# Performance work log

Hardware: AMD Instinct MI355X
Metric: run time of the kernel (lower is better)

Reference implementation:

```python
import jax, jax.numpy as jnp
import numpy as np

N, M, D, H = 16, 1024, 64, 4  # batch, num_node, dim_in==dim_hid, num_head
NEG_SLOPE = 0.2


def setup_inputs() -> dict:
    key = jax.random.key(0)
    ks = jax.random.split(key, 10)
    s = 1.0 / np.sqrt(D)
    inp = {
        "x": jax.random.normal(ks[0], (N, M, D), dtype=jnp.float32),
        "edge": jnp.zeros((N, M, M), dtype=jnp.float32),  # unused by the module
        # stacked per-head Linear(dim_in, dim_hid) params: weight (H, D_out, D_in), bias (H, D_out)
        "Wk": (jax.random.normal(ks[1], (H, D, D), dtype=jnp.float32) * s),
        "bk": (jax.random.normal(ks[2], (H, D), dtype=jnp.float32) * s),
        "Wq": (jax.random.normal(ks[3], (H, D, D), dtype=jnp.float32) * s),
        "bq": (jax.random.normal(ks[4], (H, D), dtype=jnp.float32) * s),
        "Wv": (jax.random.normal(ks[5], (H, D, D), dtype=jnp.float32) * s),
        "bv": (jax.random.normal(ks[6], (H, D), dtype=jnp.float32) * s),
        # decoder: Linear(dim_hid*num_head -> dim_in)
        "Wdec": (jax.random.normal(ks[7], (D, H * D), dtype=jnp.float32) / np.sqrt(H * D)),
        "bdec": (jax.random.normal(ks[8], (D,), dtype=jnp.float32) / np.sqrt(H * D)),
    }
    return inp


def reference(x, edge, Wk, bk, Wq, bq, Wv, bv, Wdec, bdec):
    # x: (N, M, D). Per head h: K = x @ Wk[h].T + bk[h], etc.
    K = jnp.einsum("nmd,hed->nhme", x, Wk) + bk[None, :, None, :]  # (N,H,M,D)
    Q = jnp.einsum("nmd,hed->nhme", x, Wq) + bq[None, :, None, :]
    V = jnp.einsum("nmd,hed->nhme", x, Wv) + bv[None, :, None, :]
    # alpha[n,h,i,j] = K[n,h,i] . Q[n,h,j]  (sender=K row i, receiver=Q row j)
    alpha = jnp.einsum("nhie,nhje->nhij", K, Q)  # (N,H,M,M)
    alpha = jax.nn.leaky_relu(alpha, NEG_SLOPE)
    alpha = jax.nn.softmax(alpha, axis=-1)
    agg = jnp.einsum("nhij,nhje->nhie", alpha, V)  # (N,H,M,D)
    dx = jax.nn.leaky_relu(agg, NEG_SLOPE) - x[:, None, :, :]  # (N,H,M,D)
    # concat heads along feature dim (head 0 first): (N, M, H*D)
    dx = dx.transpose(0, 2, 1, 3).reshape(N, M, H * D)
    return dx @ Wdec.T + bdec  # (N, M, D)
```

## Files before the change

### kernel.cpp

```cpp
#include <hip/hip_runtime.h>
#include <hip/hip_bf16.h>


#define NB 16
#define MM 1024
#define DD 64
#define HH 4
#define NEG 0.2f
#define AST 72
#define DST 264
#define LOG2E 1.44269504088896f

typedef __attribute__((ext_vector_type(8))) short bf16x8;
typedef __attribute__((ext_vector_type(8))) _Float16 f16x8;
typedef __attribute__((ext_vector_type(16))) float f32x16;
typedef __attribute__((ext_vector_type(4))) unsigned int uint4v;
typedef __attribute__((ext_vector_type(2))) unsigned int uint2v;

__device__ inline unsigned short f2bf(float f) {
  unsigned int u = __builtin_bit_cast(unsigned int, f);
  unsigned int r = (u + 0x7FFFu + ((u >> 16) & 1u)) >> 16;
  return (unsigned short)r;
}
__device__ inline unsigned short f2h(float f) {
  _Float16 h = (_Float16)f;
  return __builtin_bit_cast(unsigned short, h);
}
__device__ inline unsigned int pk_bf16(float lo, float hi) {
  unsigned int r;
  asm("v_cvt_pk_bf16_f32 %0, %1, %2" : "=v"(r) : "v"(lo), "v"(hi));
  return r;
}
__device__ inline void swap32(unsigned int& a, unsigned int& b) {
  uint2v r = __builtin_amdgcn_permlane32_swap(a, b, false, false);
  a = r.x;
  b = r.y;
}

__global__ __launch_bounds__(256) void prep_kernel(
    const float* __restrict__ Wk, const float* __restrict__ Wq,
    const float* __restrict__ Wv, const float* __restrict__ Wdec,
    unsigned short* __restrict__ Wf) {
  const int idx = (blockIdx.x * 256 + threadIdx.x) * 4;
  const int seg = idx >> 14, local = idx & 16383;
  const float* src = seg == 0 ? Wk : seg == 1 ? Wq : seg == 2 ? Wv : Wdec;
  float4 v = *(const float4*)&src[local];
  unsigned short p[4] = {f2h(v.x), f2h(v.y), f2h(v.z), f2h(v.w)};
  *(uint2*)&Wf[idx] = *(uint2*)p;
}

__global__ __launch_bounds__(256) void proj_kernel(
    const float* __restrict__ x, const unsigned short* __restrict__ Wf,
    const float* __restrict__ bk, const float* __restrict__ bq, const float* __restrict__ bv,
    unsigned short* __restrict__ Kf, unsigned short* __restrict__ Qf,
    unsigned short* __restrict__ Vtg) {
  __shared__ unsigned short xs[64 * AST];
  __shared__ unsigned short ob[64 * AST];
  const int t = threadIdx.x;
  const int r0 = blockIdx.x * 64;
  const int combo = blockIdx.y, mat = combo >> 2, h = combo & 3;
  const int n = r0 >> 10, ml = r0 & 1023;
  const float* bias = mat == 0 ? bk : (mat == 1 ? bq : bv);

#pragma unroll
  for (int rep = 0; rep < 2; ++rep) {
    int idx = rep * 256 + t, row = idx >> 3, c8 = (idx & 7) * 8;
    float4 a = *(const float4*)&x[(size_t)(r0 + row) * DD + c8];
    float4 b = *(const float4*)&x[(size_t)(r0 + row) * DD + c8 + 4];
    unsigned short p[8] = {f2h(a.x), f2h(a.y), f2h(a.z), f2h(a.w),
                           f2h(b.x), f2h(b.y), f2h(b.z), f2h(b.w)};
    *(uint4*)&xs[row * AST + c8] = *(uint4*)p;
  }
  __syncthreads();

  const int w = t >> 6, lane = t & 63, m31 = lane & 31, hf = lane >> 5;
  const int mi = w >> 1, ne = w & 1;
  const int ecol = h * 64 + ne * 32 + m31;
  const float bb = bias[ecol];

  f32x16 C;
#pragma unroll
  for (int r = 0; r < 16; ++r) C[r] = 0.f;
#pragma unroll
  for (int ks = 0; ks < 4; ++ks) {
    f16x8 xa = *(f16x8*)&xs[(mi * 32 + m31) * AST + ks * 16 + hf * 8];
    f16x8 wb = *(const f16x8*)&Wf[(size_t)mat * 16384 + (size_t)ecol * DD + ks * 16 + hf * 8];
    C = __builtin_amdgcn_mfma_f32_32x32x16_f16(xa, wb, C, 0, 0, 0);
  }

  if (mat < 2) {
    const float ksc = (mat == 0) ? LOG2E : 1.0f;
#pragma unroll
    for (int r = 0; r < 16; ++r) {
      int rr = (r & 3) + 8 * (r >> 2) + 4 * hf;
      ob[(mi * 32 + rr) * AST + ne * 32 + m31] = f2h((C[r] + bb) * ksc);
    }
  } else {
#pragma unroll
    for (int r = 0; r < 16; ++r) {
      int rr = (r & 3) + 8 * (r >> 2) + 4 * hf;
      ob[(ne * 32 + m31) * AST + mi * 32 + rr] = f2bf(C[r] + bb);
    }
  }
  __syncthreads();

  if (mat < 2) {
    unsigned short* dst = mat == 0 ? Kf : Qf;
    const size_t obase = (((size_t)n * HH + h) * MM + ml) * DD;
#pragma unroll
    for (int rep = 0; rep < 2; ++rep) {
      int idx = rep * 256 + t, row = idx >> 3, c8 = (idx & 7) * 8;
      *(uint4*)&dst[obase + (size_t)row * DD + c8] = *(uint4*)&ob[row * AST + c8];
    }
  } else {
    const size_t obase = (((size_t)n * HH + h) * DD) * MM + ml;
#pragma unroll
    for (int rep = 0; rep < 2; ++rep) {
      int idx = rep * 256 + t, row = idx >> 3, c8 = (idx & 7) * 8;
      *(uint4*)&Vtg[obase + (size_t)row * MM + c8] = *(uint4*)&ob[row * AST + c8];
    }
  }
}

__global__ __launch_bounds__(256, 2) void attn_kernel(
    const unsigned short* __restrict__ Kf, const unsigned short* __restrict__ Qf,
    const unsigned short* __restrict__ Vtg, const float* __restrict__ x,
    unsigned short* __restrict__ DX) {
  __shared__ __align__(16) unsigned short sm[4 * 64 * AST];
  __shared__ float ls[128];

  const int t = threadIdx.x;
  const int w = t >> 6, lane = t & 63;
  const int m31 = lane & 31, hf = lane >> 5;

  const int slot = blockIdx.x + 8 * (blockIdx.y + HH * (int)blockIdx.z);
  const int xcd = slot & 7, within = slot >> 3;
  const int grp = xcd * 8 + (within >> 3);
  const int ib = within & 7;
  const int n = grp >> 2, h = grp & 3;
  const int i0 = ib * 128;

  const size_t base = (((size_t)n * HH + h) * MM) * DD;
  const size_t baseT = (((size_t)n * HH + h) * DD) * MM;
  const unsigned short* Qp = Qf + base;
  const unsigned short* Vp = Vtg + baseT;

  f16x8 kfrag[4];
#pragma unroll
  for (int ks = 0; ks < 4; ++ks)
    kfrag[ks] = *(const f16x8*)&Kf[base + (size_t)(i0 + w * 32 + m31) * DD + ks * 16 + hf * 8];

  const int r0 = t >> 3, c8 = (t & 7) * 8;

  {
    uint4 qa = *(const uint4*)&Qp[(size_t)r0 * DD + c8];
    uint4 qb2 = *(const uint4*)&Qp[(size_t)(r0 + 32) * DD + c8];
    uint4 va = *(const uint4*)&Vp[(size_t)r0 * MM + c8];
    uint4 vb2 = *(const uint4*)&Vp[(size_t)(r0 + 32) * MM + c8];
    *(uint4*)&sm[r0 * AST + c8] = qa;
    *(uint4*)&sm[(r0 + 32) * AST + c8] = qb2;
    unsigned short* vb0 = sm + 2 * 64 * AST;
    *(uint4*)&vb0[r0 * AST + c8] = va;
    *(uint4*)&vb0[(r0 + 32) * AST + c8] = vb2;
  }
  __syncthreads();

  f32x16 agg0, agg1;
#pragma unroll
  for (int r = 0; r < 16; ++r) { agg0[r] = 0.f; agg1[r] = 0.f; }
  float lac = 0.f;

  uint4 qrA, qrB, vrA, vrB;

#pragma unroll 2
  for (int jt = 0; jt < 16; ++jt) {
    unsigned short* qb = sm + (jt & 1) * (64 * AST);
    unsigned short* vb = sm + (2 + (jt & 1)) * (64 * AST);

    if (jt < 15) {
      const int j0n = (jt + 1) * 64;
      qrA = *(const uint4*)&Qp[(size_t)(j0n + r0) * DD + c8];
      qrB = *(const uint4*)&Qp[(size_t)(j0n + r0 + 32) * DD + c8];
      vrA = *(const uint4*)&Vp[(size_t)r0 * MM + j0n + c8];
      vrB = *(const uint4*)&Vp[(size_t)(r0 + 32) * MM + j0n + c8];
    }

    bf16x8 pa[4];
#pragma unroll
    for (int tile = 0; tile < 2; ++tile) {
      f32x16 C;
#pragma unroll
      for (int r = 0; r < 16; ++r) C[r] = 0.f;
#pragma unroll
      for (int ks = 0; ks < 4; ++ks) {
        f16x8 qa = *(f16x8*)&qb[(tile * 32 + m31) * AST + ks * 16 + hf * 8];
        C = __builtin_amdgcn_mfma_f32_32x32x16_f16(qa, kfrag[ks], C, 0, 0, 0);
      }
#pragma unroll
      for (int r = 0; r < 16; ++r) {
        float s = C[r];
        s = fmaxf(s, NEG * s);
        s = __builtin_amdgcn_exp2f(s);
        lac += s;
        C[r] = s;
      }
      {
        unsigned int p01 = pk_bf16(C[0], C[1]), p23 = pk_bf16(C[2], C[3]);
        unsigned int p45 = pk_bf16(C[4], C[5]), p67 = pk_bf16(C[6], C[7]);
        swap32(p01, p45);
        swap32(p23, p67);
        uint4v wlo = {p01, p23, p45, p67};
        pa[2 * tile] = __builtin_bit_cast(bf16x8, wlo);
      }
      {
        unsigned int p89 = pk_bf16(C[8], C[9]), pAB = pk_bf16(C[10], C[11]);
        unsigned int pCD = pk_bf16(C[12], C[13]), pEF = pk_bf16(C[14], C[15]);
        swap32(p89, pCD);
        swap32(pAB, pEF);
        uint4v whi = {p89, pAB, pCD, pEF};
        pa[2 * tile + 1] = __builtin_bit_cast(bf16x8, whi);
      }
    }

#pragma unroll
    for (int ks = 0; ks < 4; ++ks) {
      bf16x8 bv0 = *(bf16x8*)&vb[m31 * AST + ks * 16 + hf * 8];
      bf16x8 bv1 = *(bf16x8*)&vb[(32 + m31) * AST + ks * 16 + hf * 8];
      agg0 = __builtin_amdgcn_mfma_f32_32x32x16_bf16(pa[ks], bv0, agg0, 0, 0, 0);
      agg1 = __builtin_amdgcn_mfma_f32_32x32x16_bf16(pa[ks], bv1, agg1, 0, 0, 0);
    }

    if (jt < 15) {
      unsigned short* qn = sm + ((jt & 1) ^ 1) * (64 * AST);
      unsigned short* vn = sm + (2 + ((jt & 1) ^ 1)) * (64 * AST);
      *(uint4*)&qn[r0 * AST + c8] = qrA;
      *(uint4*)&qn[(r0 + 32) * AST + c8] = qrB;
      *(uint4*)&vn[r0 * AST + c8] = vrA;
      *(uint4*)&vn[(r0 + 32) * AST + c8] = vrB;
    }
    __syncthreads();
  }

  const float lsum = lac + __shfl_xor(lac, 32);
  if (hf == 0) ls[w * 32 + m31] = lsum;
  __syncthreads();

#pragma unroll
  for (int r = 0; r < 16; ++r) {
    const int rr = (r & 3) + 8 * (r >> 2) + 4 * hf;
    const float rl = 1.0f / ls[w * 32 + rr];
    const size_t xrow = ((size_t)n * MM + i0 + w * 32 + rr) * DD;
    float v0 = agg0[r] * rl;
    v0 = fmaxf(v0, NEG * v0);
    v0 -= x[xrow + m31];
    sm[(w * 32 + rr) * AST + m31] = f2h(v0);
    float v1 = agg1[r] * rl;
    v1 = fmaxf(v1, NEG * v1);
    v1 -= x[xrow + 32 + m31];
    sm[(w * 32 + rr) * AST + 32 + m31] = f2h(v1);
  }
  __syncthreads();
#pragma unroll
  for (int rep = 0; rep < 4; ++rep) {
    const int idx = rep * 256 + t, row = idx >> 3, cc = (idx & 7) * 8;
    *(uint4*)&DX[((size_t)n * MM + i0 + row) * (HH * DD) + h * DD + cc] =
        *(uint4*)&sm[row * AST + cc];
  }
}

__global__ __launch_bounds__(256) void dec_kernel(
    const unsigned short* __restrict__ DX, const unsigned short* __restrict__ Wdf,
    const float* __restrict__ bdec, float* __restrict__ out) {
  __shared__ unsigned short dxs[64 * DST];
  const int t = threadIdx.x;
  const int w = t >> 6, lane = t & 63, m31 = lane & 31, hf = lane >> 5;
  const int mi = w >> 1, nd = w & 1;
  const int r0 = blockIdx.x * 64;
#pragma unroll
  for (int rep = 0; rep < 8; ++rep) {
    int idx = rep * 256 + t, row = idx >> 5, c8 = (idx & 31) * 8;
    *(uint4*)&dxs[row * DST + c8] = *(const uint4*)&DX[(size_t)(r0 + row) * 256 + c8];
  }
  __syncthreads();
  const float bb = bdec[nd * 32 + m31];
  f32x16 C;
#pragma unroll
  for (int r = 0; r < 16; ++r) C[r] = 0.f;
#pragma unroll
  for (int ks = 0; ks < 16; ++ks) {
    f16x8 aD = *(f16x8*)&dxs[(mi * 32 + m31) * DST + ks * 16 + hf * 8];
    f16x8 bW = *(const f16x8*)&Wdf[(size_t)(nd * 32 + m31) * 256 + ks * 16 + hf * 8];
    C = __builtin_amdgcn_mfma_f32_32x32x16_f16(aD, bW, C, 0, 0, 0);
  }
#pragma unroll
  for (int r = 0; r < 16; ++r) {
    int rr = (r & 3) + 8 * (r >> 2) + 4 * hf;
    out[(size_t)(r0 + mi * 32 + rr) * DD + nd * 32 + m31] = C[r] + bb;
  }
}

extern "C" void kernel_launch(void* const* d_in, const int* in_sizes, int n_in,
                              void* d_out, int out_size, void* d_ws, size_t ws_size,
                              hipStream_t stream) {
  const float* x    = (const float*)d_in[0];
  const float* Wk   = (const float*)d_in[2];
  const float* bk   = (const float*)d_in[3];
  const float* Wq   = (const float*)d_in[4];
  const float* bq   = (const float*)d_in[5];
  const float* Wv   = (const float*)d_in[6];
  const float* bv   = (const float*)d_in[7];
  const float* Wdec = (const float*)d_in[8];
  const float* bdec = (const float*)d_in[9];
  float* out = (float*)d_out;

  const size_t seg = (size_t)NB * HH * MM * DD;
  unsigned short* Kf  = (unsigned short*)d_ws;
  unsigned short* Qf  = Kf + seg;
  unsigned short* Vt  = Qf + seg;
  unsigned short* DXp = Vt + seg;
  unsigned short* Wf  = DXp + seg;
  unsigned short* Wdf = Wf + 3 * 16384;

  prep_kernel<<<64, 256, 0, stream>>>(Wk, Wq, Wv, Wdec, Wf);
  proj_kernel<<<dim3(256, 12), 256, 0, stream>>>(x, Wf, bk, bq, bv, Kf, Qf, Vt);
  attn_kernel<<<dim3(8, HH, NB), 256, 0, stream>>>(Kf, Qf, Vt, x, DXp);
  dec_kernel<<<NB * MM / 64, 256, 0, stream>>>(DXp, Wdf, bdec, out);
}
```

Measured before the change: 149.8 us.

## Software-pipeline PV MFMAs one tile behind QK to overlap softmax with matmul

```diff
diff --git a/kernel.cpp b/kernel.cpp
--- a/kernel.cpp
+++ b/kernel.cpp
@@ -8,6 +8,7 @@
 #define HH 4
 #define NEG 0.2f
 #define AST 72
+#define SLOT (64 * AST)
 #define DST 264
 #define LOG2E 1.44269504088896f
 
@@ -126,7 +127,7 @@
     const unsigned short* __restrict__ Kf, const unsigned short* __restrict__ Qf,
     const unsigned short* __restrict__ Vtg, const float* __restrict__ x,
     unsigned short* __restrict__ DX) {
-  __shared__ __align__(16) unsigned short sm[4 * 64 * AST];
+  __shared__ __align__(16) unsigned short sm[6 * SLOT];
   __shared__ float ls[128];
 
   const int t = threadIdx.x;
@@ -145,6 +146,9 @@
   const unsigned short* Qp = Qf + base;
   const unsigned short* Vp = Vtg + baseT;
 
+  unsigned short* qs = sm;
+  unsigned short* vs = sm + 2 * SLOT;
+
   f16x8 kfrag[4];
 #pragma unroll
   for (int ks = 0; ks < 4; ++ks)
@@ -157,11 +161,10 @@
     uint4 qb2 = *(const uint4*)&Qp[(size_t)(r0 + 32) * DD + c8];
     uint4 va = *(const uint4*)&Vp[(size_t)r0 * MM + c8];
     uint4 vb2 = *(const uint4*)&Vp[(size_t)(r0 + 32) * MM + c8];
-    *(uint4*)&sm[r0 * AST + c8] = qa;
-    *(uint4*)&sm[(r0 + 32) * AST + c8] = qb2;
-    unsigned short* vb0 = sm + 2 * 64 * AST;
-    *(uint4*)&vb0[r0 * AST + c8] = va;
-    *(uint4*)&vb0[(r0 + 32) * AST + c8] = vb2;
+    *(uint4*)&qs[r0 * AST + c8] = qa;
+    *(uint4*)&qs[(r0 + 32) * AST + c8] = qb2;
+    *(uint4*)&vs[r0 * AST + c8] = va;
+    *(uint4*)&vs[(r0 + 32) * AST + c8] = vb2;
   }
   __syncthreads();
 
@@ -171,29 +174,29 @@
   float lac = 0.f;
 
   uint4 qrA, qrB, vrA, vrB;
-
-#pragma unroll 2
-  for (int jt = 0; jt < 16; ++jt) {
-    unsigned short* qb = sm + (jt & 1) * (64 * AST);
-    unsigned short* vb = sm + (2 + (jt & 1)) * (64 * AST);
-
-    if (jt < 15) {
-      const int j0n = (jt + 1) * 64;
-      qrA = *(const uint4*)&Qp[(size_t)(j0n + r0) * DD + c8];
-      qrB = *(const uint4*)&Qp[(size_t)(j0n + r0 + 32) * DD + c8];
-      vrA = *(const uint4*)&Vp[(size_t)r0 * MM + j0n + c8];
-      vrB = *(const uint4*)&Vp[(size_t)(r0 + 32) * MM + j0n + c8];
-    }
-
-    bf16x8 pa[4];
-#pragma unroll
-    for (int tile = 0; tile < 2; ++tile) {
+  bf16x8 pa[2][4];
+
+  for (int g = 0; g < 4; ++g) {
+#pragma unroll
+    for (int k = 0; k < 4; ++k) {
+      const int jt = g * 4 + k;
+      unsigned short* qb = qs + (k & 1) * SLOT;
+      const bool haveNext = (k < 3) || (g < 3);
+
+      if (haveNext) {
+        const int j0n = (jt + 1) * 64;
+        qrA = *(const uint4*)&Qp[(size_t)(j0n + r0) * DD + c8];
+        qrB = *(const uint4*)&Qp[(size_t)(j0n + r0 + 32) * DD + c8];
+        vrA = *(const uint4*)&Vp[(size_t)r0 * MM + j0n + c8];
+        vrB = *(const uint4*)&Vp[(size_t)(r0 + 32) * MM + j0n + c8];
+      }
+
       f32x16 C;
 #pragma unroll
       for (int r = 0; r < 16; ++r) C[r] = 0.f;
 #pragma unroll
       for (int ks = 0; ks < 4; ++ks) {
-        f16x8 qa = *(f16x8*)&qb[(tile * 32 + m31) * AST + ks * 16 + hf * 8];
+        f16x8 qa = *(f16x8*)&qb[m31 * AST + ks * 16 + hf * 8];
         C = __builtin_amdgcn_mfma_f32_32x32x16_f16(qa, kfrag[ks], C, 0, 0, 0);
       }
 #pragma unroll
@@ -210,35 +213,77 @@
         swap32(p01, p45);
         swap32(p23, p67);
         uint4v wlo = {p01, p23, p45, p67};
-        pa[2 * tile] = __builtin_bit_cast(bf16x8, wlo);
-      }
-      {
+        pa[k & 1][0] = __builtin_bit_cast(bf16x8, wlo);
         unsigned int p89 = pk_bf16(C[8], C[9]), pAB = pk_bf16(C[10], C[11]);
         unsigned int pCD = pk_bf16(C[12], C[13]), pEF = pk_bf16(C[14], C[15]);
         swap32(p89, pCD);
         swap32(pAB, pEF);
         uint4v whi = {p89, pAB, pCD, pEF};
-        pa[2 * tile + 1] = __builtin_bit_cast(bf16x8, whi);
-      }
-    }
-
+        pa[k & 1][1] = __builtin_bit_cast(bf16x8, whi);
+      }
+
+      if ((k > 0) || (g > 0)) {
+        unsigned short* vbp = vs + ((k + 3) & 3) * SLOT;
+#pragma unroll
+        for (int ks = 0; ks < 4; ++ks) {
+          bf16x8 bv0 = *(bf16x8*)&vbp[m31 * AST + ks * 16 + hf * 8];
+          bf16x8 bv1 = *(bf16x8*)&vbp[(32 + m31) * AST + ks * 16 + hf * 8];
+          agg0 = __builtin_amdgcn_mfma_f32_32x32x16_bf16(pa[(k + 1) & 1][ks], bv0, agg0, 0, 0, 0);
+          agg1 = __builtin_amdgcn_mfma_f32_32x32x16_bf16(pa[(k + 1) & 1][ks], bv1, agg1, 0, 0, 0);
+        }
+      }
+
+#pragma unroll
+      for (int r = 0; r < 16; ++r) C[r] = 0.f;
+#pragma unroll
+      for (int ks = 0; ks < 4; ++ks) {
+        f16x8 qa = *(f16x8*)&qb[(32 + m31) * AST + ks * 16 + hf * 8];
+        C = __builtin_amdgcn_mfma_f32_32x32x16_f16(qa, kfrag[ks], C, 0, 0, 0);
+      }
+#pragma unroll
+      for (int r = 0; r < 16; ++r) {
+        float s = C[r];
+        s = fmaxf(s, NEG * s);
+        s = __builtin_amdgcn_exp2f(s);
+        lac += s;
+        C[r] = s;
+      }
+      {
+        unsigned int p01 = pk_bf16(C[0], C[1]), p23 = pk_bf16(C[2], C[3]);
+        unsigned int p45 = pk_bf16(C[4], C[5]), p67 = pk_bf16(C[6], C[7]);
+        swap32(p01, p45);
+        swap32(p23, p67);
+        uint4v wlo = {p01, p23, p45, p67};
+        pa[k & 1][2] = __builtin_bit_cast(bf16x8, wlo);
+        unsigned int p89 = pk_bf16(C[8], C[9]), pAB = pk_bf16(C[10], C[11]);
+        unsigned int pCD = pk_bf16(C[12], C[13]), pEF = pk_bf16(C[14], C[15]);
+        swap32(p89, pCD);
+        swap32(pAB, pEF);
+        uint4v whi = {p89, pAB, pCD, pEF};
+        pa[k & 1][3] = __builtin_bit_cast(bf16x8, whi);
+      }
+
+      if (haveNext) {
+        unsigned short* qn = qs + ((k + 1) & 1) * SLOT;
+        unsigned short* vn = vs + ((k + 1) & 3) * SLOT;
+        *(uint4*)&qn[r0 * AST + c8] = qrA;
+        *(uint4*)&qn[(r0 + 32) * AST + c8] = qrB;
+        *(uint4*)&vn[r0 * AST + c8] = vrA;
+        *(uint4*)&vn[(r0 + 32) * AST + c8] = vrB;
+      }
+      __syncthreads();
+    }
+  }
+
+  {
+    unsigned short* vbp = vs + 3 * SLOT;
 #pragma unroll
     for (int ks = 0; ks < 4; ++ks) {
-      bf16x8 bv0 = *(bf16x8*)&vb[m31 * AST + ks * 16 + hf * 8];
-      bf16x8 bv1 = *(bf16x8*)&vb[(32 + m31) * AST + ks * 16 + hf * 8];
-      agg0 = __builtin_amdgcn_mfma_f32_32x32x16_bf16(pa[ks], bv0, agg0, 0, 0, 0);
-      agg1 = __builtin_amdgcn_mfma_f32_32x32x16_bf16(pa[ks], bv1, agg1, 0, 0, 0);
-    }
-
-    if (jt < 15) {
-      unsigned short* qn = sm + ((jt & 1) ^ 1) * (64 * AST);
-      unsigned short* vn = sm + (2 + ((jt & 1) ^ 1)) * (64 * AST);
-      *(uint4*)&qn[r0 * AST + c8] = qrA;
-      *(uint4*)&qn[(r0 + 32) * AST + c8] = qrB;
-      *(uint4*)&vn[r0 * AST + c8] = vrA;
-      *(uint4*)&vn[(r0 + 32) * AST + c8] = vrB;
-    }
-    __syncthreads();
+      bf16x8 bv0 = *(bf16x8*)&vbp[m31 * AST + ks * 16 + hf * 8];
+      bf16x8 bv1 = *(bf16x8*)&vbp[(32 + m31) * AST + ks * 16 + hf * 8];
+      agg0 = __builtin_amdgcn_mfma_f32_32x32x16_bf16(pa[1][ks], bv0, agg0, 0, 0, 0);
+      agg1 = __builtin_amdgcn_mfma_f32_32x32x16_bf16(pa[1][ks], bv1, agg1, 0, 0, 0);
+    }
   }
 
   const float lsum = lac + __shfl_xor(lac, 32);
```

Measured after the change: 149.7 us (median of 2 runs). About the same (-0.1%).

## Store Q and V pre-swizzled in MFMA fragment order and load directly from global

Applied to the files above, without the earlier changes.

```diff
diff --git a/kernel.cpp b/kernel.cpp
--- a/kernel.cpp
+++ b/kernel.cpp
@@ -104,20 +104,30 @@
   }
   __syncthreads();
 
-  if (mat < 2) {
-    unsigned short* dst = mat == 0 ? Kf : Qf;
+  if (mat == 0) {
     const size_t obase = (((size_t)n * HH + h) * MM + ml) * DD;
 #pragma unroll
     for (int rep = 0; rep < 2; ++rep) {
       int idx = rep * 256 + t, row = idx >> 3, c8 = (idx & 7) * 8;
-      *(uint4*)&dst[obase + (size_t)row * DD + c8] = *(uint4*)&ob[row * AST + c8];
+      *(uint4*)&Kf[obase + (size_t)row * DD + c8] = *(uint4*)&ob[row * AST + c8];
+    }
+  } else if (mat == 1) {
+    const size_t obase = (((size_t)n * HH + h) * MM + ml) * DD;
+#pragma unroll
+    for (int rep = 0; rep < 2; ++rep) {
+      int idx = rep * 256 + t;
+      int jb32l = idx >> 8, ks = (idx >> 6) & 3, hf2 = (idx >> 5) & 1, mr = idx & 31;
+      *(uint4*)&Qf[obase + (size_t)idx * 8] =
+          *(uint4*)&ob[(jb32l * 32 + mr) * AST + ks * 16 + hf2 * 8];
     }
   } else {
-    const size_t obase = (((size_t)n * HH + h) * DD) * MM + ml;
+    const size_t obaseT = (((size_t)n * HH + h) * DD) * MM + (size_t)(ml >> 6) * 4096;
 #pragma unroll
     for (int rep = 0; rep < 2; ++rep) {
-      int idx = rep * 256 + t, row = idx >> 3, c8 = (idx & 7) * 8;
-      *(uint4*)&Vtg[obase + (size_t)row * MM + c8] = *(uint4*)&ob[row * AST + c8];
+      int idx = rep * 256 + t;
+      int ks = idx >> 7, eh = (idx >> 6) & 1, hf2 = (idx >> 5) & 1, mr = idx & 31;
+      *(uint4*)&Vtg[obaseT + (size_t)idx * 8] =
+          *(uint4*)&ob[(eh * 32 + mr) * AST + ks * 16 + hf2 * 8];
     }
   }
 }
@@ -126,8 +136,7 @@
     const unsigned short* __restrict__ Kf, const unsigned short* __restrict__ Qf,
     const unsigned short* __restrict__ Vtg, const float* __restrict__ x,
     unsigned short* __restrict__ DX) {
-  __shared__ __align__(16) unsigned short sm[4 * 64 * AST];
-  __shared__ float ls[128];
+  __shared__ __align__(16) unsigned short sm[128 * AST];
 
   const int t = threadIdx.x;
   const int w = t >> 6, lane = t & 63;
@@ -150,105 +159,98 @@
   for (int ks = 0; ks < 4; ++ks)
     kfrag[ks] = *(const f16x8*)&Kf[base + (size_t)(i0 + w * 32 + m31) * DD + ks * 16 + hf * 8];
 
-  const int r0 = t >> 3, c8 = (t & 7) * 8;
-
-  {
-    uint4 qa = *(const uint4*)&Qp[(size_t)r0 * DD + c8];
-    uint4 qb2 = *(const uint4*)&Qp[(size_t)(r0 + 32) * DD + c8];
-    uint4 va = *(const uint4*)&Vp[(size_t)r0 * MM + c8];
-    uint4 vb2 = *(const uint4*)&Vp[(size_t)(r0 + 32) * MM + c8];
-    *(uint4*)&sm[r0 * AST + c8] = qa;
-    *(uint4*)&sm[(r0 + 32) * AST + c8] = qb2;
-    unsigned short* vb0 = sm + 2 * 64 * AST;
-    *(uint4*)&vb0[r0 * AST + c8] = va;
-    *(uint4*)&vb0[(r0 + 32) * AST + c8] = vb2;
-  }
-  __syncthreads();
-
   f32x16 agg0, agg1;
 #pragma unroll
   for (int r = 0; r < 16; ++r) { agg0[r] = 0.f; agg1[r] = 0.f; }
   float lac = 0.f;
 
-  uint4 qrA, qrB, vrA, vrB;
+  const int loff = hf * 256 + m31 * 8;
 
 #pragma unroll 2
   for (int jt = 0; jt < 16; ++jt) {
-    unsigned short* qb = sm + (jt & 1) * (64 * AST);
-    unsigned short* vb = sm + (2 + (jt & 1)) * (64 * AST);
-
-    if (jt < 15) {
-      const int j0n = (jt + 1) * 64;
-      qrA = *(const uint4*)&Qp[(size_t)(j0n + r0) * DD + c8];
-      qrB = *(const uint4*)&Qp[(size_t)(j0n + r0 + 32) * DD + c8];
-      vrA = *(const uint4*)&Vp[(size_t)r0 * MM + j0n + c8];
-      vrB = *(const uint4*)&Vp[(size_t)(r0 + 32) * MM + j0n + c8];
+    const unsigned short* Qj = Qp + (size_t)jt * 4096;
+    const unsigned short* Vj = Vp + (size_t)jt * 4096;
+
+    f16x8 qa0[4], qa1[4];
+    bf16x8 bv0[4], bv1[4];
+#pragma unroll
+    for (int ks = 0; ks < 4; ++ks) {
+      qa0[ks] = *(const f16x8*)&Qj[ks * 512 + loff];
+      qa1[ks] = *(const f16x8*)&Qj[2048 + ks * 512 + loff];
+      bv0[ks] = *(const bf16x8*)&Vj[ks * 1024 + loff];
+      bv1[ks] = *(const bf16x8*)&Vj[ks * 1024 + 512 + loff];
     }
 
     bf16x8 pa[4];
-#pragma unroll
-    for (int tile = 0; tile < 2; ++tile) {
-      f32x16 C;
-#pragma unroll
-      for (int r = 0; r < 16; ++r) C[r] = 0.f;
-#pragma unroll
-      for (int ks = 0; ks < 4; ++ks) {
-        f16x8 qa = *(f16x8*)&qb[(tile * 32 + m31) * AST + ks * 16 + hf * 8];
-        C = __builtin_amdgcn_mfma_f32_32x32x16_f16(qa, kfrag[ks], C, 0, 0, 0);
-      }
-#pragma unroll
-      for (int r = 0; r < 16; ++r) {
-        float s = C[r];
-        s = fmaxf(s, NEG * s);
-        s = __builtin_amdgcn_exp2f(s);
-        lac += s;
-        C[r] = s;
-      }
-      {
-        unsigned int p01 = pk_bf16(C[0], C[1]), p23 = pk_bf16(C[2], C[3]);
-        unsigned int p45 = pk_bf16(C[4], C[5]), p67 = pk_bf16(C[6], C[7]);
-        swap32(p01, p45);
-        swap32(p23, p67);
-        uint4v wlo = {p01, p23, p45, p67};
-        pa[2 * tile] = __builtin_bit_cast(bf16x8, wlo);
-      }
-      {
-        unsigned int p89 = pk_bf16(C[8], C[9]), pAB = pk_bf16(C[10], C[11]);
-        unsigned int pCD = pk_bf16(C[12], C[13]), pEF = pk_bf16(C[14], C[15]);
-        swap32(p89, pCD);
-        swap32(pAB, pEF);
-        uint4v whi = {p89, pAB, pCD, pEF};
-        pa[2 * tile + 1] = __builtin_bit_cast(bf16x8, whi);
-      }
+    f32x16 C;
+#pragma unroll
+    for (int r = 0; r < 16; ++r) C[r] = 0.f;
+#pragma unroll
+    for (int ks = 0; ks < 4; ++ks)
+      C = __builtin_amdgcn_mfma_f32_32x32x16_f16(qa0[ks], kfrag[ks], C, 0, 0, 0);
+#pragma unroll
+    for (int r = 0; r < 16; ++r) {
+      float s = C[r];
+      s = fmaxf(s, NEG * s);
+      s = __builtin_amdgcn_exp2f(s);
+      lac += s;
+      C[r] = s;
+    }
+    {
+      unsigned int p01 = pk_bf16(C[0], C[1]), p23 = pk_bf16(C[2], C[3]);
+      unsigned int p45 = pk_bf16(C[4], C[5]), p67 = pk_bf16(C[6], C[7]);
+      swap32(p01, p45);
+      swap32(p23, p67);
+      uint4v wlo = {p01, p23, p45, p67};
+      pa[0] = __builtin_bit_cast(bf16x8, wlo);
+      unsigned int p89 = pk_bf16(C[8], C[9]), pAB = pk_bf16(C[10], C[11]);
+      unsigned int pCD = pk_bf16(C[12], C[13]), pEF = pk_bf16(C[14], C[15]);
+      swap32(p89, pCD);
+      swap32(pAB, pEF);
+      uint4v whi = {p89, pAB, pCD, pEF};
+      pa[1] = __builtin_bit_cast(bf16x8, whi);
+    }
+#pragma unroll
+    for (int r = 0; r < 16; ++r) C[r] = 0.f;
+#pragma unroll
+    for (int ks = 0; ks < 4; ++ks)
+      C = __builtin_amdgcn_mfma_f32_32x32x16_f16(qa1[ks], kfrag[ks], C, 0, 0, 0);
+#pragma unroll
+    for (int r = 0; r < 16; ++r) {
+      float s = C[r];
+      s = fmaxf(s, NEG * s);
+      s = __builtin_amdgcn_exp2f(s);
+      lac += s;
+      C[r] = s;
+    }
+    {
+      unsigned int p01 = pk_bf16(C[0], C[1]), p23 = pk_bf16(C[2], C[3]);
+      unsigned int p45 = pk_bf16(C[4], C[5]), p67 = pk_bf16(C[6], C[7]);
+      swap32(p01, p45);
+      swap32(p23, p67);
+      uint4v wlo = {p01, p23, p45, p67};
+      pa[2] = __builtin_bit_cast(bf16x8, wlo);
+      unsigned int p89 = pk_bf16(C[8], C[9]), pAB = pk_bf16(C[10], C[11]);
+      unsigned int pCD = pk_bf16(C[12], C[13]), pEF = pk_bf16(C[14], C[15]);
+      swap32(p89, pCD);
+      swap32(pAB, pEF);
+      uint4v whi = {p89, pAB, pCD, pEF};
+      pa[3] = __builtin_bit_cast(bf16x8, whi);
     }
 
 #pragma unroll
     for (int ks = 0; ks < 4; ++ks) {
-      bf16x8 bv0 = *(bf16x8*)&vb[m31 * AST + ks * 16 + hf * 8];
-      bf16x8 bv1 = *(bf16x8*)&vb[(32 + m31) * AST + ks * 16 + hf * 8];
-      agg0 = __builtin_amdgcn_mfma_f32_32x32x16_bf16(pa[ks], bv0, agg0, 0, 0, 0);
-      agg1 = __builtin_amdgcn_mfma_f32_32x32x16_bf16(pa[ks], bv1, agg1, 0, 0, 0);
-    }
-
-    if (jt < 15) {
-      unsigned short* qn = sm + ((jt & 1) ^ 1) * (64 * AST);
-      unsigned short* vn = sm + (2 + ((jt & 1) ^ 1)) * (64 * AST);
-      *(uint4*)&qn[r0 * AST + c8] = qrA;
-      *(uint4*)&qn[(r0 + 32) * AST + c8] = qrB;
-      *(uint4*)&vn[r0 * AST + c8] = vrA;
-      *(uint4*)&vn[(r0 + 32) * AST + c8] = vrB;
-    }
-    __syncthreads();
+      agg0 = __builtin_amdgcn_mfma_f32_32x32x16_bf16(pa[ks], bv0[ks], agg0, 0, 0, 0);
+      agg1 = __builtin_amdgcn_mfma_f32_32x32x16_bf16(pa[ks], bv1[ks], agg1, 0, 0, 0);
+    }
   }
 
   const float lsum = lac + __shfl_xor(lac, 32);
-  if (hf == 0) ls[w * 32 + m31] = lsum;
-  __syncthreads();
 
 #pragma unroll
   for (int r = 0; r < 16; ++r) {
     const int rr = (r & 3) + 8 * (r >> 2) + 4 * hf;
-    const float rl = 1.0f / ls[w * 32 + rr];
+    const float rl = 1.0f / __shfl(lsum, rr);
     const size_t xrow = ((size_t)n * MM + i0 + w * 32 + rr) * DD;
     float v0 = agg0[r] * rl;
     v0 = fmaxf(v0, NEG * v0);
```

Result: slower. 167.7 us (+11.9%).

## Split attention key dimension across two wave groups per block

Applied to the files above, without the earlier changes.

```diff
diff --git a/kernel.cpp b/kernel.cpp
--- a/kernel.cpp
+++ b/kernel.cpp
@@ -8,6 +8,7 @@
 #define HH 4
 #define NEG 0.2f
 #define AST 72
+#define SLOT (64 * AST)
 #define DST 264
 #define LOG2E 1.44269504088896f
 
@@ -122,16 +123,17 @@
   }
 }
 
-__global__ __launch_bounds__(256, 2) void attn_kernel(
+__global__ __launch_bounds__(512, 4) void attn_kernel(
     const unsigned short* __restrict__ Kf, const unsigned short* __restrict__ Qf,
     const unsigned short* __restrict__ Vtg, const float* __restrict__ x,
     unsigned short* __restrict__ DX) {
-  __shared__ __align__(16) unsigned short sm[4 * 64 * AST];
-  __shared__ float ls[128];
+  __shared__ __align__(16) unsigned short sm[8 * SLOT];
+  __shared__ float ls[2][128];
 
   const int t = threadIdx.x;
   const int w = t >> 6, lane = t & 63;
   const int m31 = lane & 31, hf = lane >> 5;
+  const int istrip = w >> 1, jh = w & 1;
 
   const int slot = blockIdx.x + 8 * (blockIdx.y + HH * (int)blockIdx.z);
   const int xcd = slot & 7, within = slot >> 3;
@@ -145,23 +147,30 @@
   const unsigned short* Qp = Qf + base;
   const unsigned short* Vp = Vtg + baseT;
 
+  unsigned short* qs = sm;
+  unsigned short* vs = sm + 4 * SLOT;
+
   f16x8 kfrag[4];
 #pragma unroll
   for (int ks = 0; ks < 4; ++ks)
-    kfrag[ks] = *(const f16x8*)&Kf[base + (size_t)(i0 + w * 32 + m31) * DD + ks * 16 + hf * 8];
-
-  const int r0 = t >> 3, c8 = (t & 7) * 8;
+    kfrag[ks] =
+        *(const f16x8*)&Kf[base + (size_t)(i0 + istrip * 32 + m31) * DD + ks * 16 + hf * 8];
+
+  const int th = t >> 8, tl = t & 255;
+  const int r0 = tl >> 3, c8 = (tl & 7) * 8;
+  const int jbase = th * 512;
 
   {
-    uint4 qa = *(const uint4*)&Qp[(size_t)r0 * DD + c8];
-    uint4 qb2 = *(const uint4*)&Qp[(size_t)(r0 + 32) * DD + c8];
-    uint4 va = *(const uint4*)&Vp[(size_t)r0 * MM + c8];
-    uint4 vb2 = *(const uint4*)&Vp[(size_t)(r0 + 32) * MM + c8];
-    *(uint4*)&sm[r0 * AST + c8] = qa;
-    *(uint4*)&sm[(r0 + 32) * AST + c8] = qb2;
-    unsigned short* vb0 = sm + 2 * 64 * AST;
-    *(uint4*)&vb0[r0 * AST + c8] = va;
-    *(uint4*)&vb0[(r0 + 32) * AST + c8] = vb2;
+    uint4 qa = *(const uint4*)&Qp[(size_t)(jbase + r0) * DD + c8];
+    uint4 qb2 = *(const uint4*)&Qp[(size_t)(jbase + r0 + 32) * DD + c8];
+    uint4 va = *(const uint4*)&Vp[(size_t)r0 * MM + jbase + c8];
+    uint4 vb2 = *(const uint4*)&Vp[(size_t)(r0 + 32) * MM + jbase + c8];
+    unsigned short* q0 = qs + (th * 2) * SLOT;
+    unsigned short* v0 = vs + (th * 2) * SLOT;
+    *(uint4*)&q0[r0 * AST + c8] = qa;
+    *(uint4*)&q0[(r0 + 32) * AST + c8] = qb2;
+    *(uint4*)&v0[r0 * AST + c8] = va;
+    *(uint4*)&v0[(r0 + 32) * AST + c8] = vb2;
   }
   __syncthreads();
 
@@ -173,12 +182,12 @@
   uint4 qrA, qrB, vrA, vrB;
 
 #pragma unroll 2
-  for (int jt = 0; jt < 16; ++jt) {
-    unsigned short* qb = sm + (jt & 1) * (64 * AST);
-    unsigned short* vb = sm + (2 + (jt & 1)) * (64 * AST);
-
-    if (jt < 15) {
-      const int j0n = (jt + 1) * 64;
+  for (int jt = 0; jt < 8; ++jt) {
+    unsigned short* qb = qs + (jh * 2 + (jt & 1)) * SLOT;
+    unsigned short* vb = vs + (jh * 2 + (jt & 1)) * SLOT;
+
+    if (jt < 7) {
+      const int j0n = jbase + (jt + 1) * 64;
       qrA = *(const uint4*)&Qp[(size_t)(j0n + r0) * DD + c8];
       qrB = *(const uint4*)&Qp[(size_t)(j0n + r0 + 32) * DD + c8];
       vrA = *(const uint4*)&Vp[(size_t)r0 * MM + j0n + c8];
@@ -211,8 +220,6 @@
         swap32(p23, p67);
         uint4v wlo = {p01, p23, p45, p67};
         pa[2 * tile] = __builtin_bit_cast(bf16x8, wlo);
-      }
-      {
         unsigned int p89 = pk_bf16(C[8], C[9]), pAB = pk_bf16(C[10], C[11]);
         unsigned int pCD = pk_bf16(C[12], C[13]), pEF = pk_bf16(C[14], C[15]);
         swap32(p89, pCD);
@@ -230,9 +237,9 @@
       agg1 = __builtin_amdgcn_mfma_f32_32x32x16_bf16(pa[ks], bv1, agg1, 0, 0, 0);
     }
 
-    if (jt < 15) {
-      unsigned short* qn = sm + ((jt & 1) ^ 1) * (64 * AST);
-      unsigned short* vn = sm + (2 + ((jt & 1) ^ 1)) * (64 * AST);
+    if (jt < 7) {
+      unsigned short* qn = qs + (th * 2 + ((jt + 1) & 1)) * SLOT;
+      unsigned short* vn = vs + (th * 2 + ((jt + 1) & 1)) * SLOT;
       *(uint4*)&qn[r0 * AST + c8] = qrA;
       *(uint4*)&qn[(r0 + 32) * AST + c8] = qrB;
       *(uint4*)&vn[r0 * AST + c8] = vrA;
@@ -242,29 +249,45 @@
   }
 
   const float lsum = lac + __shfl_xor(lac, 32);
-  if (hf == 0) ls[w * 32 + m31] = lsum;
-  __syncthreads();
-
-#pragma unroll
-  for (int r = 0; r < 16; ++r) {
-    const int rr = (r & 3) + 8 * (r >> 2) + 4 * hf;
-    const float rl = 1.0f / ls[w * 32 + rr];
-    const size_t xrow = ((size_t)n * MM + i0 + w * 32 + rr) * DD;
-    float v0 = agg0[r] * rl;
-    v0 = fmaxf(v0, NEG * v0);
-    v0 -= x[xrow + m31];
-    sm[(w * 32 + rr) * AST + m31] = f2h(v0);
-    float v1 = agg1[r] * rl;
-    v1 = fmaxf(v1, NEG * v1);
-    v1 -= x[xrow + 32 + m31];
-    sm[(w * 32 + rr) * AST + 32 + m31] = f2h(v1);
-  }
-  __syncthreads();
-#pragma unroll
-  for (int rep = 0; rep < 4; ++rep) {
-    const int idx = rep * 256 + t, row = idx >> 3, cc = (idx & 7) * 8;
+  if (hf == 0) ls[jh][istrip * 32 + m31] = lsum;
+
+  float* scratch = (float*)sm;
+  if (jh == 1) {
+#pragma unroll
+    for (int r = 0; r < 16; ++r) {
+      scratch[((istrip * 2 + 0) * 16 + r) * 64 + lane] = agg0[r];
+      scratch[((istrip * 2 + 1) * 16 + r) * 64 + lane] = agg1[r];
+    }
+  }
+  __syncthreads();
+
+  unsigned short* dxs = sm + 32768 / 2;
+  if (jh == 0) {
+#pragma unroll
+    for (int r = 0; r < 16; ++r) {
+      const int rr = (r & 3) + 8 * (r >> 2) + 4 * hf;
+      const int row = istrip * 32 + rr;
+      const float rl = 1.0f / (ls[0][row] + ls[1][row]);
+      const size_t xrow = ((size_t)n * MM + i0 + row) * DD;
+      float a0 = agg0[r] + scratch[((istrip * 2 + 0) * 16 + r) * 64 + lane];
+      float a1 = agg1[r] + scratch[((istrip * 2 + 1) * 16 + r) * 64 + lane];
+      float v0 = a0 * rl;
+      v0 = fmaxf(v0, NEG * v0);
+      v0 -= x[xrow + m31];
+      dxs[row * AST + m31] = f2h(v0);
+      float v1 = a1 * rl;
+      v1 = fmaxf(v1, NEG * v1);
+      v1 -= x[xrow + 32 + m31];
+      dxs[row * AST + 32 + m31] = f2h(v1);
+    }
+  }
+  __syncthreads();
+
+#pragma unroll
+  for (int rep = 0; rep < 2; ++rep) {
+    const int idx = rep * 512 + t, row = idx >> 3, cc = (idx & 7) * 8;
     *(uint4*)&DX[((size_t)n * MM + i0 + row) * (HH * DD) + h * DD + cc] =
-        *(uint4*)&sm[row * AST + cc];
+        *(uint4*)&dxs[row * AST + cc];
   }
 }
 
@@ -323,6 +346,6 @@
 
   prep_kernel<<<64, 256, 0, stream>>>(Wk, Wq, Wv, Wdec, Wf);
   proj_kernel<<<dim3(256, 12), 256, 0, stream>>>(x, Wf, bk, bq, bv, Kf, Qf, Vt);
-  attn_kernel<<<dim3(8, HH, NB), 256, 0, stream>>>(Kf, Qf, Vt, x, DXp);
+  attn_kernel<<<dim3(8, HH, NB), 512, 0, stream>>>(Kf, Qf, Vt, x, DXp);
   dec_kernel<<<NB * MM / 64, 256, 0, stream>>>(DXp, Wdf, bdec, out);
 }
```

Result: slower. 189.8 us (+26.7%).
